# Kernel tuning notes

Hardware: AMD Instinct MI355X
Metric: run time of the kernel (lower is better)

Reference implementation:

```python
import jax, jax.numpy as jnp
import numpy as np

B, P, D, H, L = 16384, 16, 49, 8, 6
NUM_CLASSES = 10
EPS = 1e-5


def _layernorm(x, w, b):
    mu = jnp.mean(x, axis=-1, keepdims=True)
    var = jnp.mean(jnp.square(x - mu), axis=-1, keepdims=True)
    return (x - mu) * jax.lax.rsqrt(var + EPS) * w + b


def setup_inputs() -> dict:
    key = jax.random.key(0)
    ks = iter(jax.random.split(key, 64))
    s = 0.05
    inp = {
        "x": jax.random.normal(next(ks), (B, P, D), jnp.float32),
        "trg": jax.random.randint(next(ks), (B,), 0, NUM_CLASSES, jnp.int32),
        "patch_proj_w": jax.random.normal(next(ks), (D, D)) * s,
        "patch_proj_b": jnp.zeros((D,)),
        "pos_enc": jax.random.normal(next(ks), (1, P, D)) * 0.02,
        # per-head per-layer attention weights, each head uses full dim D (as in source)
        "Wq": jax.random.normal(next(ks), (L, H, D, D)) * s,
        "bq": jnp.zeros((L, H, D)),
        "Wk": jax.random.normal(next(ks), (L, H, D, D)) * s,
        "bk": jnp.zeros((L, H, D)),
        "Wv": jax.random.normal(next(ks), (L, H, D, D)) * s,
        "bv": jnp.zeros((L, H, D)),
        "Wh": jax.random.normal(next(ks), (L, H, D, D)) * s,
        "bh": jnp.zeros((L, H, D)),
        "Wo": jax.random.normal(next(ks), (L, H * D, D)) * s,
        "bo": jnp.zeros((L, D)),
        "ln1_w": jnp.ones((L, D)), "ln1_b": jnp.zeros((L, D)),
        "ln2_w": jnp.ones((L, D)), "ln2_b": jnp.zeros((L, D)),
        "ffn1_w": jax.random.normal(next(ks), (L, D, 4 * D)) * s,
        "ffn1_b": jnp.zeros((L, 4 * D)),
        "ffn2_w": jax.random.normal(next(ks), (L, 4 * D, D)) * s,
        "ffn2_b": jnp.zeros((L, D)),
        "mlp_w1": jax.random.normal(next(ks), (D, D)) * s, "mlp_b1": jnp.zeros((D,)),
        "mlp_w2": jax.random.normal(next(ks), (D, D)) * s, "mlp_b2": jnp.zeros((D,)),
        "cls_w1": jax.random.normal(next(ks), (D, 25)) * s, "cls_b1": jnp.zeros((25,)),
        "cls_w2": jax.random.normal(next(ks), (25, NUM_CLASSES)) * s, "cls_b2": jnp.zeros((NUM_CLASSES,)),
    }
    return inp


def reference(x, trg, patch_proj_w, patch_proj_b, pos_enc,
              Wq, bq, Wk, bk, Wv, bv, Wh, bh, Wo, bo,
              ln1_w, ln1_b, ln2_w, ln2_b,
              ffn1_w, ffn1_b, ffn2_w, ffn2_b,
              mlp_w1, mlp_b1, mlp_w2, mlp_b2,
              cls_w1, cls_b1, cls_w2, cls_b2):
    b, p, d = x.shape
    h = x @ patch_proj_w + patch_proj_b + pos_enc[:, :p, :]
    scale = 1.0 / jnp.sqrt(jnp.float32(d))  # d_k = dim_proj = 49 per head
    for l in range(Wq.shape[0]):
        # all 8 heads batched: [b,p,d] x [h,d,e] -> [b,h,p,e]
        Q = jnp.einsum('bpd,hde->bhpe', h, Wq[l]) + bq[l][None, :, None, :]
        K = jnp.einsum('bpd,hde->bhpe', h, Wk[l]) + bk[l][None, :, None, :]
        V = jnp.einsum('bpd,hde->bhpe', h, Wv[l]) + bv[l][None, :, None, :]
        attn = jax.nn.softmax(jnp.einsum('bhpe,bhqe->bhpq', Q, K) * scale, axis=-1)
        ao = jnp.einsum('bhpq,bhqe->bhpe', attn, V)
        ho = jnp.einsum('bhpe,heo->bhpo', ao, Wh[l]) + bh[l][None, :, None, :]
        concat = ho.transpose(0, 2, 1, 3).reshape(b, p, -1)  # head-order concat
        attn_out = concat @ Wo[l] + bo[l]
        y = _layernorm(h + attn_out, ln1_w[l], ln1_b[l])
        ffn = jax.nn.gelu(y @ ffn1_w[l] + ffn1_b[l], approximate=False) @ ffn2_w[l] + ffn2_b[l]
        h = _layernorm(y + ffn, ln2_w[l], ln2_b[l])
        # mlp_between_blocks (shared weights) applied after every block
        h = (h @ mlp_w1 + mlp_b1) @ mlp_w2 + mlp_b2
    pooled = h.mean(axis=1)
    logits = (pooled @ cls_w1 + cls_b1) @ cls_w2 + cls_b2
    logp = jax.nn.log_softmax(logits, axis=-1)
    loss = -jnp.mean(jnp.take_along_axis(logp, trg[:, None].astype(jnp.int32), axis=-1))
    acc = jnp.mean((jnp.argmax(logits, axis=-1) == trg).astype(jnp.float32))
    return loss, acc
```

## Files before the change

### kernel.cpp

```cpp
#include <hip/hip_runtime.h>
#include <hip/hip_bf16.h>

#define DEV __device__ __forceinline__

typedef __attribute__((ext_vector_type(8))) __bf16 bfrag;
typedef __attribute__((ext_vector_type(4))) float  f32x4;
typedef __attribute__((ext_vector_type(4))) unsigned int u32x4;

DEV f32x4 mfma32(bfrag a, bfrag b, f32x4 c) {
    return __builtin_amdgcn_mfma_f32_16x16x32_bf16(a, b, c, 0, 0, 0);
}

DEV unsigned short to_bf16(float f) {
    union { __bf16 b; unsigned short u; } cv;
    cv.b = (__bf16)f;
    return cv.u;
}

DEV float bf2f(unsigned short u) {
    union { unsigned int i; float f; } cv;
    cv.i = (unsigned int)u << 16;
    return cv.f;
}

#if defined(__has_builtin)
#if __has_builtin(__builtin_amdgcn_cvt_pk_bf16_f32)
#define HAS_PK_BF16 1
#endif
#endif

DEV unsigned int pk2(float a, float b) {
#ifdef HAS_PK_BF16
    auto r = __builtin_amdgcn_cvt_pk_bf16_f32(a, b);
    unsigned int u;
    __builtin_memcpy(&u, &r, 4);
    return u;
#else
    return (unsigned)to_bf16(a) | ((unsigned)to_bf16(b) << 16);
#endif
}

DEV void store4(unsigned short* p, float v0, float v1, float v2, float v3) {
    typedef __attribute__((ext_vector_type(2))) unsigned int uint2v;
    uint2v q;
    q[0] = pk2(v0, v1);
    q[1] = pk2(v2, v3);
    *reinterpret_cast<uint2v*>(p) = q;
}

DEV bfrag bf_from(unsigned int a, unsigned int b, unsigned int c, unsigned int d) {
    u32x4 q; q[0] = a; q[1] = b; q[2] = c; q[3] = d;
    bfrag r; __builtin_memcpy(&r, &q, 16); return r;
}

DEV float fastrcp(float x) { float r; asm("v_rcp_f32 %0, %1" : "=v"(r) : "v"(x)); return r; }

DEV float gelu(float x) {
    float u = x * fmaf(0.07135481f, x * x, 1.5957691f);
    float e = __expf(-u);
    return x * fastrcp(1.0f + e);
}

namespace cfg {
constexpr size_t OFF_ACC  = 0;
constexpr size_t OFF_WQ   = 512;
constexpr size_t SZ_HEAD  = (size_t)48 * 64 * 64 * 2;
constexpr size_t OFF_WK   = OFF_WQ + SZ_HEAD;
constexpr size_t OFF_WV   = OFF_WK + SZ_HEAD;
constexpr size_t OFF_WHOO = OFF_WV + SZ_HEAD;
constexpr size_t OFF_F1   = OFF_WHOO + SZ_HEAD;
constexpr size_t OFF_F2   = OFF_F1 + (size_t)6 * 208 * 64 * 2;
constexpr size_t OFF_MF   = OFF_F2 + (size_t)6 * 64 * 224 * 2;
constexpr size_t OFF_PP   = OFF_MF + 8192;
constexpr size_t OFF_POSB = OFF_PP + 8192;
}


__global__ void pack_qk(const float* __restrict__ wq, const float* __restrict__ bq,
                        const float* __restrict__ wk, const float* __restrict__ bk,
                        char* __restrict__ ws)
{
    int id = blockIdx.x * 256 + threadIdx.x;
    int lh = id >> 12, pos = id & 4095;
    int n = pos >> 6, k = pos & 63;
    float s = 0.f;
    if (n <= 49 && k <= 49) {
        const float* aq = (n < 49) ? &wq[((size_t)lh * 49 + n) * 49] : &bq[(size_t)lh * 49];
        const float* ak = (k < 49) ? &wk[((size_t)lh * 49 + k) * 49] : &bk[(size_t)lh * 49];
        for (int e2 = 0; e2 < 49; ++e2) s += aq[e2] * ak[e2];
        s *= (1.f / 7.f);
    }
    ((unsigned short*)(ws + cfg::OFF_WQ))[(size_t)lh * 4096 + pos] = to_bf16(s);
}

__global__ void pack_v(const float* __restrict__ wv, const float* __restrict__ bv,
                       char* __restrict__ ws)
{
    int id = blockIdx.x * 256 + threadIdx.x;
    int lh = id >> 12, pos = id & 4095;
    int n = pos >> 6, k = pos & 63;
    float v = 0.f;
    if (n < 49) {
        if (k < 49)       v = wv[((size_t)lh * 49 + k) * 49 + n];
        else if (k == 49) v = bv[lh * 49 + n];
    }
    ((unsigned short*)(ws + cfg::OFF_WV))[(size_t)lh * 4096 + pos] = to_bf16(v);
}

__global__ void pack_fused(const float* __restrict__ wh, const float* __restrict__ bh,
                           const float* __restrict__ wo, const float* __restrict__ bo,
                           const float* __restrict__ m1, const float* __restrict__ m1b,
                           const float* __restrict__ m2, const float* __restrict__ m2b,
                           char* __restrict__ ws)
{
    int id = blockIdx.x * 256 + threadIdx.x;
    if (id < 48 * 4096) {
        int lh = id >> 12, pos = id & 4095;
        int l = lh >> 3, h = lh & 7;
        int d = pos >> 6, e = pos & 63;
        float s = 0.f;
        if (d < 49) {
            if (e < 49) {
                for (int o = 0; o < 49; ++o)
                    s += wh[((size_t)lh * 49 + e) * 49 + o] * wo[((size_t)l * 392 + h * 49 + o) * 49 + d];
            } else if (e == 49) {
                for (int o = 0; o < 49; ++o)
                    s += bh[lh * 49 + o] * wo[((size_t)l * 392 + h * 49 + o) * 49 + d];
                s += bo[l * 49 + d] * 0.125f;
            }
        }
        ((unsigned short*)(ws + cfg::OFF_WHOO))[(size_t)lh * 4096 + d * 64 + e] = to_bf16(s);
        return;
    }
    id -= 48 * 4096;
    if (id < 4096) {
        int d = id >> 6, e = id & 63;
        float s = 0.f;
        if (d < 49) {
            if (e < 49) {
                for (int o = 0; o < 49; ++o) s += m1[e * 49 + o] * m2[o * 49 + d];
            } else if (e == 49) {
                for (int o = 0; o < 49; ++o) s += m1b[o] * m2[o * 49 + d];
                s += m2b[d];
            }
        }
        ((unsigned short*)(ws + cfg::OFF_MF))[d * 64 + e] = to_bf16(s);
    }
}

__global__ void pack_wvo(char* __restrict__ ws)
{
    int id = blockIdx.x * 256 + threadIdx.x;
    int lh = id >> 12, pos = id & 4095;
    int d = pos >> 6, f = pos & 63;
    const unsigned short* WVp = (const unsigned short*)(ws + cfg::OFF_WV) + (size_t)lh * 4096;
    const unsigned short* WH  = (const unsigned short*)(ws + cfg::OFF_WHOO) + (size_t)lh * 4096;
    float s = 0.f;
    for (int e = 0; e < 49; ++e)
        s += bf2f(WVp[e * 64 + f]) * bf2f(WH[d * 64 + e]);
    if (f == 49) s += bf2f(WH[d * 64 + 49]);
    ((unsigned short*)(ws + cfg::OFF_WK))[(size_t)lh * 4096 + d * 64 + f] = to_bf16(s);
}

__global__ void pack_rest(const float* __restrict__ f1w, const float* __restrict__ f1b,
                          const float* __restrict__ f2w, const float* __restrict__ f2b,
                          const float* __restrict__ ppw, const float* __restrict__ ppb,
                          const float* __restrict__ pos, char* __restrict__ ws)
{
    int id = blockIdx.x * 256 + threadIdx.x;
    if (id < 6 * 208 * 64) {
        int l = id / (208 * 64), rem = id % (208 * 64), n = rem / 64, k = rem % 64;
        float v = 0.f;
        if (n < 196) {
            if (k < 49)       v = f1w[((size_t)l * 49 + k) * 196 + n];
            else if (k == 49) v = f1b[l * 196 + n];
        }
        ((unsigned short*)(ws + cfg::OFF_F1))[id] = to_bf16(v);
        return;
    }
    id -= 6 * 208 * 64;
    if (id < 6 * 64 * 224) {
        int l = id / (64 * 224), rem = id % (64 * 224), n = rem / 224, k = rem % 224;
        float v = 0.f;
        if (n < 49) {
            if (k < 196)       v = f2w[((size_t)l * 196 + k) * 49 + n];
            else if (k == 196) v = f2b[l * 49 + n];
        }
        ((unsigned short*)(ws + cfg::OFF_F2))[id] = to_bf16(v);
        return;
    }
    id -= 6 * 64 * 224;
    if (id < 4096) {
        int n = id >> 6, k = id & 63;
        ((unsigned short*)(ws + cfg::OFF_PP))[id] = to_bf16((n < 49 && k < 49) ? ppw[k * 49 + n] : 0.f);
        return;
    }
    id -= 4096;
    if (id < 1024) {
        int p = id >> 6, e = id & 63;
        ((float*)(ws + cfg::OFF_POSB))[id] = (e < 49) ? pos[p * 49 + e] + ppb[e] : 0.f;
        return;
    }
    id -= 1024;
    if (id < 128) ((float*)(ws + cfg::OFF_ACC))[id] = 0.f;
}


__global__ __launch_bounds__(128, 2)
void vit_main(const float* __restrict__ x, const int* __restrict__ trg,
              const float* __restrict__ cw1, const float* __restrict__ cb1,
              const float* __restrict__ cw2, const float* __restrict__ cb2,
              char* __restrict__ ws)
{
    constexpr int S64 = 72;
    constexpr int VC  = 36;
    constexpr int TA = 0, TB = 1152, EL = 2304;
    __shared__ unsigned short smb[4 * EL];

    const int tid  = threadIdx.x;
    const int wid  = tid >> 6;
    const int lane = tid & 63;
    const int g = lane >> 4, c = lane & 15;
    const long e0 = (long)blockIdx.x * 4 + wid * 2;
    unsigned short* const sm = smb + wid * 2 * EL;
    const f32x4 FZ = {0.f, 0.f, 0.f, 0.f};

    const int src0 = ((( 2 * g )     & 3) << 4) | c;
    const int src1 = (((2 * g + 1) & 3) << 4) | c;
    const bool glo = (g < 2);

    const unsigned short* WQK = (const unsigned short*)(ws + cfg::OFF_WQ);
    const unsigned short* WVO = (const unsigned short*)(ws + cfg::OFF_WK);
    const unsigned short* F1 = (const unsigned short*)(ws + cfg::OFF_F1);
    const unsigned short* F2 = (const unsigned short*)(ws + cfg::OFF_F2);
    const unsigned short* MF = (const unsigned short*)(ws + cfg::OFF_MF);
    const unsigned short* PP = (const unsigned short*)(ws + cfg::OFF_PP);
    const float* POSB = (const float*)(ws + cfg::OFF_POSB);
    float* ACC = (float*)(ws + cfg::OFF_ACC);

    #pragma unroll
    for (int u = 0; u < 2; ++u) {
        const float* xb = x + (e0 + u) * 784;
        #pragma unroll
        for (int it = 0; it < 8; ++it) {
            int i = it * 64 + lane;
            int p = i >> 5, ee = (i & 31) * 2;
            float v0 = (ee < 49) ? xb[p * 49 + ee] : 0.f;
            float v1 = (ee + 1 < 49) ? xb[p * 49 + ee + 1] : 0.f;
            *reinterpret_cast<unsigned int*>(&sm[u * EL + TA + p * S64 + ee]) = pk2(v0, v1);
        }
    }

    bfrag a_h[2][2];
    auto loadB = [&](int off, bfrag (&af)[2][2]) {
        #pragma unroll
        for (int u = 0; u < 2; ++u)
            #pragma unroll
            for (int kk = 0; kk < 2; ++kk)
                af[u][kk] = *(const bfrag*)&sm[u * EL + off + c * S64 + kk * 32 + g * 8];
    };
    loadB(TA, a_h);

    f32x4 hreg[2][4];
    #pragma unroll
    for (int mt = 0; mt < 4; ++mt) {
        f32x4 t0 = FZ, t1 = FZ;
        #pragma unroll
        for (int kk = 0; kk < 2; ++kk) {
            bfrag w = *(const bfrag*)&PP[(mt * 16 + c) * 64 + kk * 32 + g * 8];
            t0 = mfma32(w, a_h[0][kk], t0);
            t1 = mfma32(w, a_h[1][kk], t1);
        }
        f32x4 pb = *(const f32x4*)&POSB[c * 64 + mt * 16 + 4 * g];
        hreg[0][mt] = t0 + pb;
        hreg[1][mt] = t1 + pb;
    }

    for (int l = 0; l < 6; ++l) {
        #pragma unroll
        for (int u = 0; u < 2; ++u)
            #pragma unroll
            for (int mt = 0; mt < 4; ++mt)
                store4(&sm[u * EL + TA + c * S64 + mt * 16 + 4 * g],
                       hreg[u][mt][0], hreg[u][mt][1], hreg[u][mt][2], hreg[u][mt][3]);
        if (lane < 32) sm[(lane >> 4) * EL + TA + (lane & 15) * S64 + 49] = 0x3F80;
        loadB(TA, a_h);

        f32x4 oacc[2][4];
        #pragma unroll
        for (int u = 0; u < 2; ++u)
            #pragma unroll
            for (int mt = 0; mt < 4; ++mt) oacc[u][mt] = FZ;

        for (int hh = 0; hh < 8; ++hh) {
            const int lh = l * 8 + hh;
            const unsigned short* wqk = WQK + (size_t)lh * 4096;
            const unsigned short* wvo = WVO + (size_t)lh * 4096;

            #pragma unroll
            for (int mt = 0; mt < 4; ++mt) {
                f32x4 t0 = FZ, t1 = FZ;
                #pragma unroll
                for (int kk = 0; kk < 2; ++kk) {
                    bfrag wf = *(const bfrag*)&wqk[(mt * 16 + c) * 64 + kk * 32 + g * 8];
                    t0 = mfma32(wf, a_h[0][kk], t0);
                    t1 = mfma32(wf, a_h[1][kk], t1);
                }
                store4(&sm[0 * EL + TB + c * S64 + mt * 16 + 4 * g], t0[0], t0[1], t0[2], t0[3]);
                store4(&sm[1 * EL + TB + c * S64 + mt * 16 + 4 * g], t1[0], t1[1], t1[2], t1[3]);
            }

            bfrag bp[2];
            #pragma unroll
            for (int u = 0; u < 2; ++u) {
                f32x4 sc = FZ;
                #pragma unroll
                for (int kk = 0; kk < 2; ++kk) {
                    bfrag akf = *(const bfrag*)&sm[u * EL + TB + c * S64 + kk * 32 + g * 8];
                    sc = mfma32(akf, a_h[u][kk], sc);
                }
                float s0 = sc[0], s1 = sc[1], s2 = sc[2], s3 = sc[3];
                float m = fmaxf(fmaxf(s0, s1), fmaxf(s2, s3));
                m = fmaxf(m, __shfl_xor(m, 16));
                m = fmaxf(m, __shfl_xor(m, 32));
                float p0 = __expf(s0 - m), p1 = __expf(s1 - m);
                float p2 = __expf(s2 - m), p3 = __expf(s3 - m);
                float t = p0 + p1 + p2 + p3;
                t += __shfl_xor(t, 16);
                t += __shfl_xor(t, 32);
                float inv = fastrcp(t);
                unsigned int pka = pk2(p0 * inv, p1 * inv);
                unsigned int pkb = pk2(p2 * inv, p3 * inv);
                unsigned int b0 = (unsigned)__shfl((int)pka, src0);
                unsigned int b1 = (unsigned)__shfl((int)pkb, src0);
                unsigned int b2 = (unsigned)__shfl((int)pka, src1);
                unsigned int b3 = (unsigned)__shfl((int)pkb, src1);
                bp[u] = bf_from(glo ? b0 : 0u, glo ? b1 : 0u,
                                glo ? b2 : 0u, glo ? b3 : 0u);
            }

            #pragma unroll
            for (int nt = 0; nt < 4; ++nt) {
                bfrag wvf0 = *(const bfrag*)&wvo[(nt * 16 + c) * 64 + 0 * 32 + g * 8];
                bfrag wvf1 = *(const bfrag*)&wvo[(nt * 16 + c) * 64 + 1 * 32 + g * 8];
                #pragma unroll
                for (int u = 0; u < 2; ++u) {
                    f32x4 v = FZ;
                    v = mfma32(a_h[u][0], wvf0, v);
                    v = mfma32(a_h[u][1], wvf1, v);
                    unsigned int va = pk2(v[0], v[1]);
                    unsigned int vb = pk2(v[2], v[3]);
                    unsigned int u0 = (unsigned)__shfl((int)va, src0);
                    unsigned int u1 = (unsigned)__shfl((int)vb, src0);
                    unsigned int u2 = (unsigned)__shfl((int)va, src1);
                    unsigned int u3 = (unsigned)__shfl((int)vb, src1);
                    bfrag uf = bf_from(glo ? u0 : 0u, glo ? u1 : 0u,
                                       glo ? u2 : 0u, glo ? u3 : 0u);
                    oacc[u][nt] = mfma32(uf, bp[u], oacc[u][nt]);
                }
            }
        }

        f32x4 yreg[2][4];
        {
            const float* ln1wp = (const float*)(ws + cfg::OFF_POSB + 4096);
            const float* ln1bp = ln1wp + 384;
            #pragma unroll
            for (int u = 0; u < 2; ++u) {
                float z[4][4];
                float s = 0.f, q2 = 0.f;
                #pragma unroll
                for (int mt = 0; mt < 4; ++mt)
                    #pragma unroll
                    for (int r = 0; r < 4; ++r) {
                        float zz = hreg[u][mt][r] + oacc[u][mt][r];
                        z[mt][r] = zz;
                        s += zz;
                        q2 += zz * zz;
                    }
                s += __shfl_xor(s, 16); s += __shfl_xor(s, 32);
                q2 += __shfl_xor(q2, 16); q2 += __shfl_xor(q2, 32);
                float mu = s * (1.f / 49.f);
                float var = q2 * (1.f / 49.f) - mu * mu;
                float rstd = rsqrtf(var + 1e-5f);
                #pragma unroll
                for (int mt = 0; mt < 4; ++mt) {
                    f32x4 lwv = *(const f32x4*)&ln1wp[l * 64 + mt * 16 + 4 * g];
                    f32x4 lbv = *(const f32x4*)&ln1bp[l * 64 + mt * 16 + 4 * g];
                    #pragma unroll
                    for (int r = 0; r < 4; ++r)
                        yreg[u][mt][r] = (z[mt][r] - mu) * rstd * lwv[r] + lbv[r];
                    store4(&sm[u * EL + TA + c * S64 + mt * 16 + 4 * g],
                           yreg[u][mt][0], yreg[u][mt][1], yreg[u][mt][2], yreg[u][mt][3]);
                }
            }
        }
        if (lane < 32) sm[(lane >> 4) * EL + TA + (lane & 15) * S64 + 49] = 0x3F80;

        f32x4 zac[2][4];
        #pragma unroll
        for (int u = 0; u < 2; ++u)
            #pragma unroll
            for (int mt = 0; mt < 4; ++mt) zac[u][mt] = FZ;
        {
            bfrag ay[2][2];
            loadB(TA, ay);
            const unsigned short* F1l = F1 + (size_t)l * 208 * 64;
            const unsigned short* F2l = F2 + (size_t)l * 64 * 224;
            #pragma unroll
            for (int ci = 0; ci < 7; ++ci) {
                #pragma unroll
                for (int t = 0; t < 2; ++t) {
                    const int mtile = ci * 2 + t;
                    if (mtile < 13) {
                        f32x4 m0 = FZ, m1 = FZ;
                        #pragma unroll
                        for (int kk = 0; kk < 2; ++kk) {
                            bfrag wf = *(const bfrag*)&F1l[(mtile * 16 + c) * 64 + kk * 32 + g * 8];
                            m0 = mfma32(wf, ay[0][kk], m0);
                            m1 = mfma32(wf, ay[1][kk], m1);
                        }
                        store4(&sm[0 * EL + TB + c * VC + t * 16 + 4 * g],
                               gelu(m0[0]), gelu(m0[1]), gelu(m0[2]), gelu(m0[3]));
                        store4(&sm[1 * EL + TB + c * VC + t * 16 + 4 * g],
                               gelu(m1[0]), gelu(m1[1]), gelu(m1[2]), gelu(m1[3]));
                    } else {
                        int u2 = lane >> 5, r5 = lane & 31, row = r5 >> 1, half = r5 & 1;
                        *(f32x4*)&sm[u2 * EL + TB + row * VC + 16 + half * 8] = FZ;
                    }
                }
                if (ci == 6) {
                    if (lane < 32) sm[(lane >> 4) * EL + TB + (lane & 15) * VC + 4] = 0x3F80;
                }
                #pragma unroll
                for (int u = 0; u < 2; ++u) {
                    bfrag am = *(const bfrag*)&sm[u * EL + TB + c * VC + g * 8];
                    #pragma unroll
                    for (int mt = 0; mt < 4; ++mt) {
                        bfrag wf = *(const bfrag*)&F2l[(mt * 16 + c) * 224 + ci * 32 + g * 8];
                        zac[u][mt] = mfma32(wf, am, zac[u][mt]);
                    }
                }
            }
        }

        {
            const float* ln2wp = (const float*)(ws + cfg::OFF_POSB + 4096) + 768;
            const float* ln2bp = ln2wp + 384;
            #pragma unroll
            for (int u = 0; u < 2; ++u) {
                float z[4][4];
                float s = 0.f, q2 = 0.f;
                #pragma unroll
                for (int mt = 0; mt < 4; ++mt)
                    #pragma unroll
                    for (int r = 0; r < 4; ++r) {
                        float zz = yreg[u][mt][r] + zac[u][mt][r];
                        z[mt][r] = zz;
                        s += zz;
                        q2 += zz * zz;
                    }
                s += __shfl_xor(s, 16); s += __shfl_xor(s, 32);
                q2 += __shfl_xor(q2, 16); q2 += __shfl_xor(q2, 32);
                float mu = s * (1.f / 49.f);
                float var = q2 * (1.f / 49.f) - mu * mu;
                float rstd = rsqrtf(var + 1e-5f);
                #pragma unroll
                for (int mt = 0; mt < 4; ++mt) {
                    f32x4 lwv = *(const f32x4*)&ln2wp[l * 64 + mt * 16 + 4 * g];
                    f32x4 lbv = *(const f32x4*)&ln2bp[l * 64 + mt * 16 + 4 * g];
                    #pragma unroll
                    for (int r = 0; r < 4; ++r)
                        hreg[u][mt][r] = (z[mt][r] - mu) * rstd * lwv[r] + lbv[r];
                    store4(&sm[u * EL + TA + c * S64 + mt * 16 + 4 * g],
                           hreg[u][mt][0], hreg[u][mt][1], hreg[u][mt][2], hreg[u][mt][3]);
                }
            }
        }
        if (lane < 32) sm[(lane >> 4) * EL + TA + (lane & 15) * S64 + 49] = 0x3F80;

        {
            bfrag an[2][2];
            loadB(TA, an);
            #pragma unroll
            for (int mt = 0; mt < 4; ++mt) {
                f32x4 t0 = FZ, t1 = FZ;
                #pragma unroll
                for (int kk = 0; kk < 2; ++kk) {
                    bfrag wf = *(const bfrag*)&MF[(mt * 16 + c) * 64 + kk * 32 + g * 8];
                    t0 = mfma32(wf, an[0][kk], t0);
                    t1 = mfma32(wf, an[1][kk], t1);
                }
                hreg[0][mt] = t0;
                hreg[1][mt] = t1;
            }
        }
    }

    float loss_blk = 0.f, corr_blk = 0.f;
    #pragma unroll
    for (int u = 0; u < 2; ++u)
        #pragma unroll
        for (int mt = 0; mt < 4; ++mt)
            store4(&sm[u * EL + TA + c * S64 + mt * 16 + 4 * g],
                   hreg[u][mt][0], hreg[u][mt][1], hreg[u][mt][2], hreg[u][mt][3]);

    for (int u = 0; u < 2; ++u) {
        float s = 0.f;
        #pragma unroll
        for (int p = 0; p < 16; ++p)
            s += (float)(*reinterpret_cast<const __bf16*>(&sm[u * EL + TA + p * S64 + lane]));
        float* pf = reinterpret_cast<float*>(&sm[u * EL + TB]);
        pf[lane] = s * (1.f / 16.f);
        if (lane < 25) {
            float t = cb1[lane];
            for (int d2 = 0; d2 < 49; ++d2) t += pf[d2] * cw1[d2 * 25 + lane];
            pf[64 + lane] = t;
        }
        if (lane < 10) {
            float t2 = cb2[lane];
            for (int k2 = 0; k2 < 25; ++k2) t2 += pf[64 + k2] * cw2[k2 * 10 + lane];
            pf[96 + lane] = t2;
        }
        if (lane == 0) {
            float m = pf[96]; int am_ = 0;
            for (int j = 1; j < 10; ++j) if (pf[96 + j] > m) { m = pf[96 + j]; am_ = j; }
            float se = 0.f;
            for (int j = 0; j < 10; ++j) se += __expf(pf[96 + j] - m);
            float logZ = m + logf(se);
            int t = trg[e0 + u];
            loss_blk += logZ - pf[96 + t];
            corr_blk += (am_ == t) ? 1.f : 0.f;
        }
    }
    if (lane == 0) {
        int bin = (int)((blockIdx.x * 2 + wid) & 63);
        atomicAdd(&ACC[bin * 2 + 0], loss_blk);
        atomicAdd(&ACC[bin * 2 + 1], corr_blk);
    }
}

__global__ void pack_ln(const float* __restrict__ ln1w, const float* __restrict__ ln1b,
                        const float* __restrict__ ln2w, const float* __restrict__ ln2b,
                        char* __restrict__ ws)
{
    int id = blockIdx.x * 256 + threadIdx.x;
    if (id >= 1536) return;
    int which = id / 384, r = id % 384, l = r >> 6, f = r & 63;
    const float* s = (which == 0) ? ln1w : (which == 1) ? ln1b : (which == 2) ? ln2w : ln2b;
    float v = (f < 49) ? s[l * 49 + f] : 0.f;
    ((float*)(ws + cfg::OFF_POSB + 4096))[which * 384 + r] = v;
}

__global__ void finalize_k(const char* __restrict__ ws, float* __restrict__ out)
{
    const float* ACC = (const float*)(ws + cfg::OFF_ACC);
    int lane = threadIdx.x;
    float a = ACC[lane * 2 + 0];
    float b = ACC[lane * 2 + 1];
    for (int m = 1; m < 64; m <<= 1) {
        a += __shfl_xor(a, m);
        b += __shfl_xor(b, m);
    }
    if (lane == 0) {
        out[0] = a * (1.f / 16384.f);
        out[1] = b * (1.f / 16384.f);
    }
}


extern "C" void kernel_launch(void* const* d_in, const int* in_sizes, int n_in,
                              void* d_out, int out_size, void* d_ws, size_t ws_size,
                              hipStream_t stream)
{
    const float* x    = (const float*)d_in[0];
    const int*   trg  = (const int*)  d_in[1];
    const float* ppw  = (const float*)d_in[2];
    const float* ppb  = (const float*)d_in[3];
    const float* pos  = (const float*)d_in[4];
    const float* wq   = (const float*)d_in[5];
    const float* bq   = (const float*)d_in[6];
    const float* wk   = (const float*)d_in[7];
    const float* bk   = (const float*)d_in[8];
    const float* wv   = (const float*)d_in[9];
    const float* bv   = (const float*)d_in[10];
    const float* wh   = (const float*)d_in[11];
    const float* bh   = (const float*)d_in[12];
    const float* wo   = (const float*)d_in[13];
    const float* bo   = (const float*)d_in[14];
    const float* ln1w = (const float*)d_in[15];
    const float* ln1b = (const float*)d_in[16];
    const float* ln2w = (const float*)d_in[17];
    const float* ln2b = (const float*)d_in[18];
    const float* f1w  = (const float*)d_in[19];
    const float* f1b  = (const float*)d_in[20];
    const float* f2w  = (const float*)d_in[21];
    const float* f2b  = (const float*)d_in[22];
    const float* m1w  = (const float*)d_in[23];
    const float* m1b  = (const float*)d_in[24];
    const float* m2w  = (const float*)d_in[25];
    const float* m2b  = (const float*)d_in[26];
    const float* cw1  = (const float*)d_in[27];
    const float* cb1  = (const float*)d_in[28];
    const float* cw2  = (const float*)d_in[29];
    const float* cb2  = (const float*)d_in[30];
    char* ws = (char*)d_ws;

    pack_qk<<<768, 256, 0, stream>>>(wq, bq, wk, bk, ws);
    pack_v<<<768, 256, 0, stream>>>(wv, bv, ws);
    pack_fused<<<784, 256, 0, stream>>>(wh, bh, wo, bo, m1w, m1b, m2w, m2b, ws);
    pack_wvo<<<768, 256, 0, stream>>>(ws);
    pack_rest<<<669, 256, 0, stream>>>(f1w, f1b, f2w, f2b, ppw, ppb, pos, ws);
    pack_ln<<<6, 256, 0, stream>>>(ln1w, ln1b, ln2w, ln2b, ws);
    vit_main<<<16384 / 4, 128, 0, stream>>>(x, trg, cw1, cb1, cw2, cb2, ws);
    finalize_k<<<1, 64, 0, stream>>>(ws, (float*)d_out);
}
```

Before: 1.188 ms.

## Double-buffer per-head QK/VO weights in LDS via async global_load_lds

Per-head fused QK and VO bf16 weights are now staged into a double-buffered LDS region with async global_load_lds, prefetching the next head while the current one computes. MFMA operand loads then read from LDS instead of global memory. This adds a block-wide barrier per head and 32KB of extra LDS, which may lower occupancy under launch_bounds(128,2). There is no explicit wait on the async loads (vmcnt) before the barrier, so correctness depends on the compiler or barrier draining them.

```diff
diff --git a/kernel.cpp b/kernel.cpp
--- a/kernel.cpp
+++ b/kernel.cpp
@@ -215,7 +215,7 @@
     constexpr int S64 = 72;
     constexpr int VC  = 36;
     constexpr int TA = 0, TB = 1152, EL = 2304;
-    __shared__ unsigned short smb[4 * EL];
+    __shared__ unsigned short smb[4 * EL + 16384];
 
     const int tid  = threadIdx.x;
     const int wid  = tid >> 6;
@@ -223,14 +223,13 @@
     const int g = lane >> 4, c = lane & 15;
     const long e0 = (long)blockIdx.x * 4 + wid * 2;
     unsigned short* const sm = smb + wid * 2 * EL;
+    unsigned short* const wbuf = smb + 4 * EL;
     const f32x4 FZ = {0.f, 0.f, 0.f, 0.f};
 
     const int src0 = ((( 2 * g )     & 3) << 4) | c;
     const int src1 = (((2 * g + 1) & 3) << 4) | c;
     const bool glo = (g < 2);
 
-    const unsigned short* WQK = (const unsigned short*)(ws + cfg::OFF_WQ);
-    const unsigned short* WVO = (const unsigned short*)(ws + cfg::OFF_WK);
     const unsigned short* F1 = (const unsigned short*)(ws + cfg::OFF_F1);
     const unsigned short* F2 = (const unsigned short*)(ws + cfg::OFF_F2);
     const unsigned short* MF = (const unsigned short*)(ws + cfg::OFF_MF);
@@ -238,6 +237,23 @@
     const float* POSB = (const float*)(ws + cfg::OFF_POSB);
     float* ACC = (float*)(ws + cfg::OFF_ACC);
 
+    const char* const WQKb = (const char*)ws + cfg::OFF_WQ;
+    const char* const WVOb = (const char*)ws + cfg::OFF_WK;
+    auto stage = [&](int buf, int lh) {
+        char* dstb = (char*)wbuf + (buf << 14);
+        #pragma unroll
+        for (int t = 0; t < 8; ++t) {
+            int j = wid * 8 + t;
+            const char* src = ((j < 8) ? WQKb + (size_t)lh * 8192 + (j << 10)
+                                       : WVOb + (size_t)lh * 8192 + ((j - 8) << 10))
+                              + lane * 16;
+            __builtin_amdgcn_global_load_lds(
+                (const __attribute__((address_space(1))) unsigned int*)src,
+                (__attribute__((address_space(3))) unsigned int*)(dstb + (j << 10)),
+                16, 0, 0);
+        }
+    };
+
     #pragma unroll
     for (int u = 0; u < 2; ++u) {
         const float* xb = x + (e0 + u) * 784;
@@ -250,6 +266,8 @@
             *reinterpret_cast<unsigned int*>(&sm[u * EL + TA + p * S64 + ee]) = pk2(v0, v1);
         }
     }
+    stage(0, 0);
+    __syncthreads();
 
     bfrag a_h[2][2];
     auto loadB = [&](int off, bfrag (&af)[2][2]) {
@@ -293,16 +311,23 @@
             for (int mt = 0; mt < 4; ++mt) oacc[u][mt] = FZ;
 
         for (int hh = 0; hh < 8; ++hh) {
-            const int lh = l * 8 + hh;
-            const unsigned short* wqk = WQK + (size_t)lh * 4096;
-            const unsigned short* wvo = WVO + (size_t)lh * 4096;
+            const int cur = hh & 1;
+            {
+                int nlh = (hh < 7) ? (l * 8 + hh + 1) : ((l < 5) ? (l + 1) * 8 : -1);
+                if (nlh >= 0) {
+                    stage(cur ^ 1, nlh);
+                    __builtin_amdgcn_sched_barrier(0);
+                }
+            }
+            const unsigned short* wq_l = wbuf + (cur << 13);
+            const unsigned short* wv_l = wq_l + 4096;
 
             #pragma unroll
             for (int mt = 0; mt < 4; ++mt) {
                 f32x4 t0 = FZ, t1 = FZ;
                 #pragma unroll
                 for (int kk = 0; kk < 2; ++kk) {
-                    bfrag wf = *(const bfrag*)&wqk[(mt * 16 + c) * 64 + kk * 32 + g * 8];
+                    bfrag wf = *(const bfrag*)&wq_l[(mt * 16 + c) * 64 + kk * 32 + g * 8];
                     t0 = mfma32(wf, a_h[0][kk], t0);
                     t1 = mfma32(wf, a_h[1][kk], t1);
                 }
@@ -341,8 +366,8 @@
 
             #pragma unroll
             for (int nt = 0; nt < 4; ++nt) {
-                bfrag wvf0 = *(const bfrag*)&wvo[(nt * 16 + c) * 64 + 0 * 32 + g * 8];
-                bfrag wvf1 = *(const bfrag*)&wvo[(nt * 16 + c) * 64 + 1 * 32 + g * 8];
+                bfrag wvf0 = *(const bfrag*)&wv_l[(nt * 16 + c) * 64 + 0 * 32 + g * 8];
+                bfrag wvf1 = *(const bfrag*)&wv_l[(nt * 16 + c) * 64 + 1 * 32 + g * 8];
                 #pragma unroll
                 for (int u = 0; u < 2; ++u) {
                     f32x4 v = FZ;
@@ -359,6 +384,8 @@
                     oacc[u][nt] = mfma32(uf, bp[u], oacc[u][nt]);
                 }
             }
+
+            __syncthreads();
         }
 
         f32x4 yreg[2][4];
```

After: 1.217 ms. 2.5% more time.
